# Kernel tuning notes

Hardware: AMD Instinct MI355X
Metric: run time of the kernel (lower is better)

Reference implementation:

```python
import jax, jax.numpy as jnp
import numpy as np

EPS = 1e-12  # torch F.normalize eps


def _l2norm(v, axis):
    n = jnp.sqrt(jnp.sum(v * v, axis=axis, keepdims=True))
    return v / jnp.maximum(n, EPS)


def setup_inputs() -> dict:
    key = jax.random.key(0)
    k1, k2, k3 = jax.random.split(key, 3)
    N, C, H, W = 32, 512, 60, 60
    K = 64
    x = jax.random.normal(k1, (N, C, H, W), dtype=jnp.float32)
    conv_w = jax.random.normal(k2, (K, C), dtype=jnp.float32) * 0.05
    centroids = jax.random.uniform(k3, (K, C), dtype=jnp.float32)
    return {"x": x, "conv_w": conv_w, "centroids": centroids}


def reference(x, conv_w, centroids):
    N, C = x.shape[:2]
    K = centroids.shape[0]
    # descriptor-wise L2 normalization over channel dim
    xn = _l2norm(x, axis=1)
    xf = xn.reshape(N, C, -1)              # [N, C, S]
    # 1x1 conv == per-pixel matmul with weight [K, C]
    logits = jnp.einsum('kc,ncs->nks', conv_w, xf)   # [N, K, S]
    a = jax.nn.softmax(logits, axis=1)               # softmax over clusters
    # vlad[n,k,c] = sum_s a[n,k,s] * (xf[n,c,s] - centroids[k,c])
    agg = jnp.einsum('nks,ncs->nkc', a, xf)          # [N, K, C]
    vlad = agg - a.sum(axis=-1)[:, :, None] * centroids[None, :, :]
    # intra-normalization then global L2
    vlad = _l2norm(vlad, axis=2)
    vlad = vlad.reshape(N, -1)
    vlad = _l2norm(vlad, axis=1)
    return vlad
```

## Files before the change

kernel.cpp:

```cpp
#include <hip/hip_runtime.h>
#include <math.h>

#define EPS 1e-12f
#define NN 32
#define CDIM 512
#define SDIM 3600
#define KDIM 64

__global__ __launch_bounds__(256) void k0_transpose(
    const float* __restrict__ w, float* __restrict__ wT)
{
  int i = blockIdx.x * 256 + threadIdx.x;
  int k = i >> 9;
  int c = i & 511;
  wT[c * KDIM + k] = w[i];
}

__device__ __forceinline__ void k1_finish(
    float* acc, float nrm, int n, int s, bool valid,
    float* __restrict__ a, float* __restrict__ invn_out)
{
  float invn = 1.f / fmaxf(sqrtf(nrm), EPS);
  float m = acc[0];
  #pragma unroll
  for (int k = 1; k < 64; ++k) m = fmaxf(m, acc[k]);
  float sum = 0.f;
  #pragma unroll
  for (int k = 0; k < 64; ++k) {
    float e = __expf((acc[k] - m) * invn);
    acc[k] = e;
    sum += e;
  }
  float rs = 1.f / sum;
  if (valid) {
    float* ap = a + (size_t)n * KDIM * SDIM + s;
    #pragma unroll
    for (int k = 0; k < 64; ++k) ap[(size_t)k * SDIM] = acc[k] * rs;
    invn_out[n * SDIM + s] = invn;
  }
}

__global__ __launch_bounds__(128) void k1_softmax(
    const float* __restrict__ x, const float* __restrict__ wT,
    float* __restrict__ a, float* __restrict__ invn_out)
{
  __shared__ float wt[64 * 64];
  const int n = blockIdx.y;
  const int s0r = blockIdx.x * 256 + threadIdx.x;
  const int s1r = s0r + 128;
  const bool v0 = s0r < SDIM, v1 = s1r < SDIM;
  const int s0 = v0 ? s0r : (SDIM - 1);
  const int s1 = v1 ? s1r : (SDIM - 1);
  const float* xb = x + (size_t)n * CDIM * SDIM;
  const float* xp0 = xb + s0;
  const float* xp1 = xb + s1;

  float acc0[64], acc1[64];
  #pragma unroll
  for (int k = 0; k < 64; ++k) { acc0[k] = 0.f; acc1[k] = 0.f; }
  float nrm0 = 0.f, nrm1 = 0.f;

  for (int c0 = 0; c0 < CDIM; c0 += 64) {
    __syncthreads();
    const float4* src = (const float4*)(wT + c0 * 64);
    float4* dst = (float4*)wt;
    for (int i = threadIdx.x; i < 1024; i += 128) dst[i] = src[i];
    __syncthreads();

    for (int cc = 0; cc < 64; ++cc) {
      float xv0 = xp0[(size_t)(c0 + cc) * SDIM];
      float xv1 = xp1[(size_t)(c0 + cc) * SDIM];
      nrm0 = fmaf(xv0, xv0, nrm0);
      nrm1 = fmaf(xv1, xv1, nrm1);
      const float4* wr = (const float4*)(&wt[cc * 64]);
      #pragma unroll
      for (int q = 0; q < 16; ++q) {
        float4 w4 = wr[q];
        acc0[q * 4 + 0] = fmaf(w4.x, xv0, acc0[q * 4 + 0]);
        acc0[q * 4 + 1] = fmaf(w4.y, xv0, acc0[q * 4 + 1]);
        acc0[q * 4 + 2] = fmaf(w4.z, xv0, acc0[q * 4 + 2]);
        acc0[q * 4 + 3] = fmaf(w4.w, xv0, acc0[q * 4 + 3]);
        acc1[q * 4 + 0] = fmaf(w4.x, xv1, acc1[q * 4 + 0]);
        acc1[q * 4 + 1] = fmaf(w4.y, xv1, acc1[q * 4 + 1]);
        acc1[q * 4 + 2] = fmaf(w4.z, xv1, acc1[q * 4 + 2]);
        acc1[q * 4 + 3] = fmaf(w4.w, xv1, acc1[q * 4 + 3]);
      }
    }
  }

  k1_finish(acc0, nrm0, n, s0, v0, a, invn_out);
  k1_finish(acc1, nrm1, n, s1, v1, a, invn_out);
}

__global__ __launch_bounds__(256) void k2_agg(
    const float* __restrict__ a, const float* __restrict__ x,
    const float* __restrict__ invn, float* __restrict__ aggp)
{
  __shared__ float xs[60 * 132];
  __shared__ float at[60 * 72];
  const int n = blockIdx.y;
  const int c0 = blockIdx.x * 128;
  const int sbase = blockIdx.z * 900;
  const int tk = threadIdx.x >> 4;
  const int tc = threadIdx.x & 15;

  float acc[32];
  #pragma unroll
  for (int i = 0; i < 32; ++i) acc[i] = 0.f;

  for (int ch = 0; ch < 15; ++ch) {
    const int ss = sbase + ch * 60;
    __syncthreads();
    for (int i = threadIdx.x; i < 7680; i += 256) {
      int c = i / 60;
      int s = i - c * 60;
      xs[s * 132 + c] = x[((size_t)n * CDIM + c0 + c) * SDIM + ss + s] *
                        invn[n * SDIM + ss + s];
    }
    for (int i = threadIdx.x; i < 3840; i += 256) {
      int k = i / 60;
      int s = i - k * 60;
      at[s * 72 + k] = a[((size_t)n * KDIM + k) * SDIM + ss + s];
    }
    __syncthreads();
    #pragma unroll 4
    for (int s = 0; s < 60; ++s) {
      float4 av  = *(const float4*)(&at[s * 72 + tk * 4]);
      float4 xv0 = *(const float4*)(&xs[s * 132 + tc * 4]);
      float4 xv1 = *(const float4*)(&xs[s * 132 + 64 + tc * 4]);
      #pragma unroll
      for (int j = 0; j < 4; ++j) {
        float aj = (j == 0) ? av.x : (j == 1) ? av.y : (j == 2) ? av.z : av.w;
        acc[j * 8 + 0] = fmaf(aj, xv0.x, acc[j * 8 + 0]);
        acc[j * 8 + 1] = fmaf(aj, xv0.y, acc[j * 8 + 1]);
        acc[j * 8 + 2] = fmaf(aj, xv0.z, acc[j * 8 + 2]);
        acc[j * 8 + 3] = fmaf(aj, xv0.w, acc[j * 8 + 3]);
        acc[j * 8 + 4] = fmaf(aj, xv1.x, acc[j * 8 + 4]);
        acc[j * 8 + 5] = fmaf(aj, xv1.y, acc[j * 8 + 5]);
        acc[j * 8 + 6] = fmaf(aj, xv1.z, acc[j * 8 + 6]);
        acc[j * 8 + 7] = fmaf(aj, xv1.w, acc[j * 8 + 7]);
      }
    }
  }

  float* outp = aggp + ((size_t)blockIdx.z * NN + n) * KDIM * CDIM;
  #pragma unroll
  for (int j = 0; j < 4; ++j) {
    int k = tk * 4 + j;
    *(float4*)(&outp[(size_t)k * CDIM + c0 + tc * 4]) =
        make_float4(acc[j*8+0], acc[j*8+1], acc[j*8+2], acc[j*8+3]);
    *(float4*)(&outp[(size_t)k * CDIM + c0 + 64 + tc * 4]) =
        make_float4(acc[j*8+4], acc[j*8+5], acc[j*8+6], acc[j*8+7]);
  }
}

__global__ __launch_bounds__(256) void k3_finalize(
    const float* __restrict__ a, const float* __restrict__ aggp,
    const float* __restrict__ cent, float* __restrict__ out,
    float* __restrict__ gsum)
{
  const int k = blockIdx.x;
  const int n = blockIdx.y;
  __shared__ float red[16];

  float p = 0.f;
  const float* ap = a + ((size_t)n * KDIM + k) * SDIM;
  for (int s = threadIdx.x; s < SDIM; s += 256) p += ap[s];
  #pragma unroll
  for (int o = 32; o > 0; o >>= 1) p += __shfl_xor(p, o);
  int wid = threadIdx.x >> 6;
  if ((threadIdx.x & 63) == 0) red[wid] = p;
  __syncthreads();
  float asum = red[0] + red[1] + red[2] + red[3];

  float v[2];
  float ss_ = 0.f;
  #pragma unroll
  for (int r = 0; r < 2; ++r) {
    int c = r * 256 + threadIdx.x;
    float t = 0.f;
    #pragma unroll
    for (int sp = 0; sp < 4; ++sp)
      t += aggp[(((size_t)sp * NN + n) * KDIM + k) * CDIM + c];
    t -= asum * cent[k * CDIM + c];
    v[r] = t;
    ss_ = fmaf(t, t, ss_);
  }
  #pragma unroll
  for (int o = 32; o > 0; o >>= 1) ss_ += __shfl_xor(ss_, o);
  if ((threadIdx.x & 63) == 0) red[8 + wid] = ss_;
  __syncthreads();
  float rowss = red[8] + red[9] + red[10] + red[11];

  float scale = 1.f / fmaxf(sqrtf(rowss), EPS);
  #pragma unroll
  for (int r = 0; r < 2; ++r)
    out[((size_t)n * KDIM + k) * CDIM + r * 256 + threadIdx.x] = v[r] * scale;
  if (threadIdx.x == 0) atomicAdd(&gsum[n], rowss * scale * scale);
}

__global__ __launch_bounds__(256) void k4_scale(
    float* __restrict__ out, const float* __restrict__ gsum)
{
  const int n = blockIdx.y;
  const float g = 1.f / fmaxf(sqrtf(gsum[n]), EPS);
  size_t base = (size_t)n * KDIM * CDIM + (size_t)blockIdx.x * 1024 + threadIdx.x * 4;
  float4* p = (float4*)(out + base);
  float4 vv = *p;
  vv.x *= g; vv.y *= g; vv.z *= g; vv.w *= g;
  *p = vv;
}

extern "C" void kernel_launch(void* const* d_in, const int* in_sizes, int n_in,
                              void* d_out, int out_size, void* d_ws, size_t ws_size,
                              hipStream_t stream) {
  const float* x    = (const float*)d_in[0];
  const float* w    = (const float*)d_in[1];
  const float* cent = (const float*)d_in[2];
  float* out = (float*)d_out;
  float* ws = (float*)d_ws;

  float* a    = ws;
  float* invn = a + (size_t)NN * KDIM * SDIM;
  float* aggp = invn + (size_t)NN * SDIM;
  float* gsum = aggp + (size_t)4 * NN * KDIM * CDIM;
  float* wT   = gsum + 64;

  hipMemsetAsync(gsum, 0, NN * sizeof(float), stream);

  k0_transpose<<<dim3(128), 256, 0, stream>>>(w, wT);
  k1_softmax  <<<dim3(15, 32), 128, 0, stream>>>(x, wT, a, invn);
  k2_agg      <<<dim3(4, 32, 4), 256, 0, stream>>>(a, x, invn, aggp);
  k3_finalize <<<dim3(64, 32), 256, 0, stream>>>(a, aggp, cent, out, gsum);
  k4_scale    <<<dim3(32, 32), 256, 0, stream>>>(out, gsum);
}
```

Baseline: 838.5 us.

## Halve per-thread work in softmax and aggregation kernels, stage x via LDS

The softmax kernel now uses 256 threads with one pixel per thread, which halves the accumulator registers from 128 to 64. It stages 32-channel tiles of x into shared memory with float4 coalesced loads instead of strided scalar global reads. The aggregation kernel narrows its channel tile from 128 to 64 and doubles its grid, so each thread holds 16 accumulators instead of 32. The aim is more occupancy and parallelism, at the cost of less register-level reuse and more redundant loads of the a tile in k2.

```diff
diff --git a/kernel.cpp b/kernel.cpp
--- a/kernel.cpp
+++ b/kernel.cpp
@@ -16,10 +16,74 @@
   wT[c * KDIM + k] = w[i];
 }
 
-__device__ __forceinline__ void k1_finish(
-    float* acc, float nrm, int n, int s, bool valid,
+__global__ __launch_bounds__(256) void k1_softmax(
+    const float* __restrict__ x, const float* __restrict__ wT,
     float* __restrict__ a, float* __restrict__ invn_out)
 {
+  __shared__ float xs[32 * 256];
+  __shared__ float wt[32 * 64];
+  const int n = blockIdx.y;
+  const int sbase = blockIdx.x * 256;
+  const int tid = threadIdx.x;
+  const int s_raw = sbase + tid;
+  const bool valid = s_raw < SDIM;
+  const float* xb = x + (size_t)n * CDIM * SDIM;
+  const bool full = (sbase + 256) <= SDIM;
+
+  float acc[64];
+  #pragma unroll
+  for (int k = 0; k < 64; ++k) acc[k] = 0.f;
+  float nrm = 0.f;
+
+  for (int c0 = 0; c0 < CDIM; c0 += 32) {
+    __syncthreads();
+    {
+      const float4* src = (const float4*)(wT + c0 * 64);
+      float4* dst = (float4*)wt;
+      dst[tid]       = src[tid];
+      dst[tid + 256] = src[tid + 256];
+    }
+    if (full) {
+      #pragma unroll
+      for (int it = 0; it < 8; ++it) {
+        int idx = tid + it * 256;
+        int cc  = idx >> 6;
+        int f4  = idx & 63;
+        float4 v = *(const float4*)(xb + (size_t)(c0 + cc) * SDIM + sbase + f4 * 4);
+        *(float4*)(&xs[cc * 256 + f4 * 4]) = v;
+      }
+    } else {
+      #pragma unroll
+      for (int it = 0; it < 8; ++it) {
+        int idx = tid + it * 256;
+        int cc  = idx >> 6;
+        int f4  = idx & 63;
+        #pragma unroll
+        for (int j = 0; j < 4; ++j) {
+          int s = sbase + f4 * 4 + j;
+          xs[cc * 256 + f4 * 4 + j] =
+              (s < SDIM) ? xb[(size_t)(c0 + cc) * SDIM + s] : 0.f;
+        }
+      }
+    }
+    __syncthreads();
+
+    #pragma unroll 2
+    for (int cc = 0; cc < 32; ++cc) {
+      float xv = xs[cc * 256 + tid];
+      nrm = fmaf(xv, xv, nrm);
+      const float4* wr = (const float4*)(&wt[cc * 64]);
+      #pragma unroll
+      for (int q = 0; q < 16; ++q) {
+        float4 w4 = wr[q];
+        acc[q * 4 + 0] = fmaf(w4.x, xv, acc[q * 4 + 0]);
+        acc[q * 4 + 1] = fmaf(w4.y, xv, acc[q * 4 + 1]);
+        acc[q * 4 + 2] = fmaf(w4.z, xv, acc[q * 4 + 2]);
+        acc[q * 4 + 3] = fmaf(w4.w, xv, acc[q * 4 + 3]);
+      }
+    }
+  }
+
   float invn = 1.f / fmaxf(sqrtf(nrm), EPS);
   float m = acc[0];
   #pragma unroll
@@ -32,90 +96,39 @@
     sum += e;
   }
   float rs = 1.f / sum;
+
   if (valid) {
-    float* ap = a + (size_t)n * KDIM * SDIM + s;
+    float* ap = a + (size_t)n * KDIM * SDIM + s_raw;
     #pragma unroll
     for (int k = 0; k < 64; ++k) ap[(size_t)k * SDIM] = acc[k] * rs;
-    invn_out[n * SDIM + s] = invn;
-  }
-}
-
-__global__ __launch_bounds__(128) void k1_softmax(
-    const float* __restrict__ x, const float* __restrict__ wT,
-    float* __restrict__ a, float* __restrict__ invn_out)
-{
-  __shared__ float wt[64 * 64];
-  const int n = blockIdx.y;
-  const int s0r = blockIdx.x * 256 + threadIdx.x;
-  const int s1r = s0r + 128;
-  const bool v0 = s0r < SDIM, v1 = s1r < SDIM;
-  const int s0 = v0 ? s0r : (SDIM - 1);
-  const int s1 = v1 ? s1r : (SDIM - 1);
-  const float* xb = x + (size_t)n * CDIM * SDIM;
-  const float* xp0 = xb + s0;
-  const float* xp1 = xb + s1;
-
-  float acc0[64], acc1[64];
-  #pragma unroll
-  for (int k = 0; k < 64; ++k) { acc0[k] = 0.f; acc1[k] = 0.f; }
-  float nrm0 = 0.f, nrm1 = 0.f;
-
-  for (int c0 = 0; c0 < CDIM; c0 += 64) {
-    __syncthreads();
-    const float4* src = (const float4*)(wT + c0 * 64);
-    float4* dst = (float4*)wt;
-    for (int i = threadIdx.x; i < 1024; i += 128) dst[i] = src[i];
-    __syncthreads();
-
-    for (int cc = 0; cc < 64; ++cc) {
-      float xv0 = xp0[(size_t)(c0 + cc) * SDIM];
-      float xv1 = xp1[(size_t)(c0 + cc) * SDIM];
-      nrm0 = fmaf(xv0, xv0, nrm0);
-      nrm1 = fmaf(xv1, xv1, nrm1);
-      const float4* wr = (const float4*)(&wt[cc * 64]);
-      #pragma unroll
-      for (int q = 0; q < 16; ++q) {
-        float4 w4 = wr[q];
-        acc0[q * 4 + 0] = fmaf(w4.x, xv0, acc0[q * 4 + 0]);
-        acc0[q * 4 + 1] = fmaf(w4.y, xv0, acc0[q * 4 + 1]);
-        acc0[q * 4 + 2] = fmaf(w4.z, xv0, acc0[q * 4 + 2]);
-        acc0[q * 4 + 3] = fmaf(w4.w, xv0, acc0[q * 4 + 3]);
-        acc1[q * 4 + 0] = fmaf(w4.x, xv1, acc1[q * 4 + 0]);
-        acc1[q * 4 + 1] = fmaf(w4.y, xv1, acc1[q * 4 + 1]);
-        acc1[q * 4 + 2] = fmaf(w4.z, xv1, acc1[q * 4 + 2]);
-        acc1[q * 4 + 3] = fmaf(w4.w, xv1, acc1[q * 4 + 3]);
-      }
-    }
-  }
-
-  k1_finish(acc0, nrm0, n, s0, v0, a, invn_out);
-  k1_finish(acc1, nrm1, n, s1, v1, a, invn_out);
+    invn_out[n * SDIM + s_raw] = invn;
+  }
 }
 
 __global__ __launch_bounds__(256) void k2_agg(
     const float* __restrict__ a, const float* __restrict__ x,
     const float* __restrict__ invn, float* __restrict__ aggp)
 {
-  __shared__ float xs[60 * 132];
+  __shared__ float xs[60 * 68];
   __shared__ float at[60 * 72];
   const int n = blockIdx.y;
-  const int c0 = blockIdx.x * 128;
+  const int c0 = blockIdx.x * 64;
   const int sbase = blockIdx.z * 900;
   const int tk = threadIdx.x >> 4;
   const int tc = threadIdx.x & 15;
 
-  float acc[32];
-  #pragma unroll
-  for (int i = 0; i < 32; ++i) acc[i] = 0.f;
+  float acc[16];
+  #pragma unroll
+  for (int i = 0; i < 16; ++i) acc[i] = 0.f;
 
   for (int ch = 0; ch < 15; ++ch) {
     const int ss = sbase + ch * 60;
     __syncthreads();
-    for (int i = threadIdx.x; i < 7680; i += 256) {
+    for (int i = threadIdx.x; i < 3840; i += 256) {
       int c = i / 60;
       int s = i - c * 60;
-      xs[s * 132 + c] = x[((size_t)n * CDIM + c0 + c) * SDIM + ss + s] *
-                        invn[n * SDIM + ss + s];
+      xs[s * 68 + c] = x[((size_t)n * CDIM + c0 + c) * SDIM + ss + s] *
+                       invn[n * SDIM + ss + s];
     }
     for (int i = threadIdx.x; i < 3840; i += 256) {
       int k = i / 60;
@@ -125,21 +138,24 @@
     __syncthreads();
     #pragma unroll 4
     for (int s = 0; s < 60; ++s) {
-      float4 av  = *(const float4*)(&at[s * 72 + tk * 4]);
-      float4 xv0 = *(const float4*)(&xs[s * 132 + tc * 4]);
-      float4 xv1 = *(const float4*)(&xs[s * 132 + 64 + tc * 4]);
-      #pragma unroll
-      for (int j = 0; j < 4; ++j) {
-        float aj = (j == 0) ? av.x : (j == 1) ? av.y : (j == 2) ? av.z : av.w;
-        acc[j * 8 + 0] = fmaf(aj, xv0.x, acc[j * 8 + 0]);
-        acc[j * 8 + 1] = fmaf(aj, xv0.y, acc[j * 8 + 1]);
-        acc[j * 8 + 2] = fmaf(aj, xv0.z, acc[j * 8 + 2]);
-        acc[j * 8 + 3] = fmaf(aj, xv0.w, acc[j * 8 + 3]);
-        acc[j * 8 + 4] = fmaf(aj, xv1.x, acc[j * 8 + 4]);
-        acc[j * 8 + 5] = fmaf(aj, xv1.y, acc[j * 8 + 5]);
-        acc[j * 8 + 6] = fmaf(aj, xv1.z, acc[j * 8 + 6]);
-        acc[j * 8 + 7] = fmaf(aj, xv1.w, acc[j * 8 + 7]);
-      }
+      float4 av = *(const float4*)(&at[s * 72 + tk * 4]);
+      float4 xv = *(const float4*)(&xs[s * 68 + tc * 4]);
+      acc[ 0] = fmaf(av.x, xv.x, acc[ 0]);
+      acc[ 1] = fmaf(av.x, xv.y, acc[ 1]);
+      acc[ 2] = fmaf(av.x, xv.z, acc[ 2]);
+      acc[ 3] = fmaf(av.x, xv.w, acc[ 3]);
+      acc[ 4] = fmaf(av.y, xv.x, acc[ 4]);
+      acc[ 5] = fmaf(av.y, xv.y, acc[ 5]);
+      acc[ 6] = fmaf(av.y, xv.z, acc[ 6]);
+      acc[ 7] = fmaf(av.y, xv.w, acc[ 7]);
+      acc[ 8] = fmaf(av.z, xv.x, acc[ 8]);
+      acc[ 9] = fmaf(av.z, xv.y, acc[ 9]);
+      acc[10] = fmaf(av.z, xv.z, acc[10]);
+      acc[11] = fmaf(av.z, xv.w, acc[11]);
+      acc[12] = fmaf(av.w, xv.x, acc[12]);
+      acc[13] = fmaf(av.w, xv.y, acc[13]);
+      acc[14] = fmaf(av.w, xv.z, acc[14]);
+      acc[15] = fmaf(av.w, xv.w, acc[15]);
     }
   }
 
@@ -148,9 +164,7 @@
   for (int j = 0; j < 4; ++j) {
     int k = tk * 4 + j;
     *(float4*)(&outp[(size_t)k * CDIM + c0 + tc * 4]) =
-        make_float4(acc[j*8+0], acc[j*8+1], acc[j*8+2], acc[j*8+3]);
-    *(float4*)(&outp[(size_t)k * CDIM + c0 + 64 + tc * 4]) =
-        make_float4(acc[j*8+4], acc[j*8+5], acc[j*8+6], acc[j*8+7]);
+        make_float4(acc[j*4+0], acc[j*4+1], acc[j*4+2], acc[j*4+3]);
   }
 }
 
@@ -229,8 +243,8 @@
   hipMemsetAsync(gsum, 0, NN * sizeof(float), stream);
 
   k0_transpose<<<dim3(128), 256, 0, stream>>>(w, wT);
-  k1_softmax  <<<dim3(15, 32), 128, 0, stream>>>(x, wT, a, invn);
-  k2_agg      <<<dim3(4, 32, 4), 256, 0, stream>>>(a, x, invn, aggp);
+  k1_softmax  <<<dim3(15, 32), 256, 0, stream>>>(x, wT, a, invn);
+  k2_agg      <<<dim3(8, 32, 4), 256, 0, stream>>>(a, x, invn, aggp);
   k3_finalize <<<dim3(64, 32), 256, 0, stream>>>(a, aggp, cent, out, gsum);
   k4_scale    <<<dim3(32, 32), 256, 0, stream>>>(out, gsum);
 }
```

Result: faster. 806.7 us (-3.8%).
